# Optimization experiments

Hardware: AMD Instinct MI355X
Metric: run time of the kernel (lower is better)

The kernel has to match this reference:

```python
import jax, jax.numpy as jnp
import numpy as np

N, F = 4096, 256  # nodes, in_features == hidden_features == out_features; num_heads = 1
LN_EPS = 1e-5
L1_EPS = 1e-12


def setup_inputs() -> dict:
    key = jax.random.key(0)
    k0, k1, k2, k3, k4 = jax.random.split(key, 5)
    h = jax.random.normal(k0, (N, F), jnp.float32)
    x = jax.random.normal(k1, (N, F), jnp.float32)
    s = 1.0 / np.sqrt(F)
    s_v = 1.0 / np.sqrt(F + 3)
    # torch Linear weight layout: [out_features, in_features]
    w_k = jax.random.uniform(k2, (F, F), jnp.float32, -s, s)
    w_q = jax.random.uniform(k3, (F, F), jnp.float32, -s, s)
    w_v = jax.random.uniform(k4, (F, F + 3), jnp.float32, -s_v, s_v)
    # mixing init: ones * semantic_weight(-1.0), row 0 zeroed
    mixing = jnp.full((2, 2), -1.0, jnp.float32).at[0].set(0.0)
    ln_gamma = jnp.ones((F,), jnp.float32)
    ln_beta = jnp.zeros((F,), jnp.float32)
    return {"h": h, "x": x, "w_k": w_k, "w_q": w_q, "w_v": w_v,
            "mixing": mixing, "ln_gamma": ln_gamma, "ln_beta": ln_beta}


def reference(h, x, w_k, w_q, w_v, mixing, ln_gamma, ln_beta):
    h0, x0 = h, x
    # LayerNorm (biased variance, eps=1e-5)
    mu = h.mean(-1, keepdims=True)
    var = ((h - mu) ** 2).mean(-1, keepdims=True)
    hn = (h - mu) * jax.lax.rsqrt(var + LN_EPS) * ln_gamma + ln_beta
    # F.normalize(x, p=1): divide by max(L1 norm, eps)
    xn = x / jnp.maximum(jnp.abs(x).sum(-1, keepdims=True), L1_EPS)
    # projections (single head: [N, F])
    k = hn @ w_k.T
    q = hn @ w_q.T
    # feature-attention: softmax over last dim of k q^T / sqrt(F)
    a_h = jax.nn.softmax((k @ q.T) * (F ** -0.5), axis=-1)          # [N, N]
    # x-affinity
    a_x = xn @ xn.T                                                  # [N, N]
    # stats of a_x rows: diag, sum, std (unbiased, ddof=1)
    i = jnp.stack([jnp.diagonal(a_x), a_x.sum(-1), a_x.std(-1, ddof=1)], axis=-1)  # [N, 3]
    # learned 2x2 mixing, softmax over dim 0 (columns)
    m = jax.nn.softmax(mixing, axis=0)
    a_x2 = a_x * m[0, 0] + a_h * m[1, 0]
    a_h2 = a_x * m[0, 1] + a_h * m[1, 1]
    # torch a_h.transpose(-1, 0) swaps the row axis with the head axis,
    # transposing the NxN matrix (head dim = 1): h <- a_h2^T @ hn
    h_agg = a_h2.T @ hn                                              # [N, F]
    x_out = a_x2 @ xn                                                # [N, F]
    h_out = jax.nn.elu(jnp.concatenate([h_agg, i], axis=-1) @ w_v.T)
    return (h_out + h0, x_out + x0)
```

## Files before the change

### kernel.cpp

```cpp
#include <hip/hip_runtime.h>
#include <cstdint>
#include <cstddef>

#define NB 4096
#define FD 256

typedef __attribute__((ext_vector_type(4))) float f32x4;
typedef __attribute__((ext_vector_type(8))) short bf16x8;

__device__ __forceinline__ ushort f2bf(float f) {
  union { float f; uint32_t u; } v; v.f = f;
  uint32_t r = v.u + 0x7fffu + ((v.u >> 16) & 1u);
  return (ushort)(r >> 16);
}
__device__ __forceinline__ float bf2f(ushort b) {
  union { uint32_t u; float f; } v; v.u = ((uint32_t)b) << 16;
  return v.f;
}

__device__ __forceinline__ void gld16(const void* g, void* l) {
  __builtin_amdgcn_global_load_lds(
      (const __attribute__((address_space(1))) char*)g,
      (__attribute__((address_space(3))) char*)l, 16, 0, 0);
}

__device__ __forceinline__ float wave_reduce_sum(float v) {
#pragma unroll
  for (int off = 32; off >= 1; off >>= 1) v += __shfl_xor(v, off);
  return v;
}
__device__ __forceinline__ float wave_reduce_max(float v) {
#pragma unroll
  for (int off = 32; off >= 1; off >>= 1) v = fmaxf(v, __shfl_xor(v, off));
  return v;
}

__global__ __launch_bounds__(256) void rownorm_wcast_kernel(
    const float* __restrict__ h, const float* __restrict__ x,
    const float* __restrict__ gamma, const float* __restrict__ beta,
    ushort* __restrict__ hnb, ushort* __restrict__ xnb, float* __restrict__ diag,
    const float* __restrict__ w_k, const float* __restrict__ w_q,
    const float* __restrict__ w_v,
    ushort* __restrict__ wkqb, ushort* __restrict__ wvAb,
    float* __restrict__ wvbT3) {
  __shared__ float rA[4], rB[4], rC[4], rD[4];
  if (blockIdx.x >= NB) {
    const int r = blockIdx.x - NB, t = threadIdx.x;
    wkqb[r * 256 + t] = f2bf(w_k[r * 256 + t]);
    wkqb[(256 + r) * 256 + t] = f2bf(w_q[r * 256 + t]);
    wvAb[r * 256 + t] = f2bf(w_v[(size_t)r * 259 + t]);
    if (t < 3) wvbT3[t * 256 + r] = w_v[(size_t)r * 259 + 256 + t];
    return;
  }
  const int r = blockIdx.x, t = threadIdx.x, wid = t >> 6, lane = t & 63;
  const size_t base = (size_t)r * FD + t;
  const float hv = h[base], xv = x[base];
  float s1 = wave_reduce_sum(hv);
  float s2 = wave_reduce_sum(hv * hv);
  float a1 = wave_reduce_sum(fabsf(xv));
  float q1 = wave_reduce_sum(xv * xv);
  if (lane == 0) { rA[wid] = s1; rB[wid] = s2; rC[wid] = a1; rD[wid] = q1; }
  __syncthreads();
  const float S1 = rA[0] + rA[1] + rA[2] + rA[3];
  const float S2 = rB[0] + rB[1] + rB[2] + rB[3];
  const float L1 = rC[0] + rC[1] + rC[2] + rC[3];
  const float Q1 = rD[0] + rD[1] + rD[2] + rD[3];
  const float mu = S1 * (1.0f / FD);
  const float var = S2 * (1.0f / FD) - mu * mu;
  const float rstd = rsqrtf(var + 1e-5f);
  const float d = fmaxf(L1, 1e-12f), dinv = 1.0f / d;
  hnb[base] = f2bf((hv - mu) * rstd * gamma[t] + beta[t]);
  xnb[base] = f2bf(xv * dinv);
  if (t == 0) diag[r] = Q1 * dinv * dinv;
}

__global__ __launch_bounds__(256) void transpose2_kernel(
    const ushort* __restrict__ inA, ushort* __restrict__ outA,
    const ushort* __restrict__ inB, ushort* __restrict__ outB, int R, int C) {
  __shared__ ushort tile[64][65];
  const ushort* in = blockIdx.z ? inB : inA;
  ushort* out = blockIdx.z ? outB : outA;
  const int bc = blockIdx.x * 64, br = blockIdx.y * 64;
  const int t = threadIdx.x;
#pragma unroll
  for (int i = 0; i < 16; ++i) {
    const int idx = t + 256 * i;
    const int rr = idx >> 6, cc = idx & 63;
    tile[rr][cc] = in[(size_t)(br + rr) * C + bc + cc];
  }
  __syncthreads();
#pragma unroll
  for (int i = 0; i < 16; ++i) {
    const int idx = t + 256 * i;
    const int rr = idx >> 6, cc = idx & 63;
    out[(size_t)(bc + rr) * R + br + cc] = tile[cc][rr];
  }
}

__global__ __launch_bounds__(256) void transpose4_kernel(
    const ushort* __restrict__ in, ushort* __restrict__ out, int R, int C) {
  __shared__ ushort tile[64][66];
  const int bc = blockIdx.x * 64, br = blockIdx.y * 64;
  const int t = threadIdx.x;
  const int c4 = (t & 15) * 4;
  const int r0 = t >> 4;
#pragma unroll
  for (int i = 0; i < 4; ++i) {
    const int rr = r0 + 16 * i;
    *(ushort4*)&tile[rr][c4] =
        *(const ushort4*)(in + (size_t)(br + rr) * C + bc + c4);
  }
  __syncthreads();
#pragma unroll
  for (int i = 0; i < 4; ++i) {
    const int ro = r0 + 16 * i;
    ushort4 o;
    o.x = tile[c4 + 0][ro];
    o.y = tile[c4 + 1][ro];
    o.z = tile[c4 + 2][ro];
    o.w = tile[c4 + 3][ro];
    *(ushort4*)(out + (size_t)(bc + ro) * R + br + c4) = o;
  }
}

__global__ __launch_bounds__(256) void colsum_kernel(
    const ushort* __restrict__ xnT, float* __restrict__ s) {
  __shared__ float red[4];
  const int f = blockIdx.x, t = threadIdx.x, wid = t >> 6, lane = t & 63;
  float a = 0.f;
#pragma unroll
  for (int i = 0; i < 16; ++i) a += bf2f(xnT[(size_t)f * NB + t + 256 * i]);
  a = wave_reduce_sum(a);
  if (lane == 0) red[wid] = a;
  __syncthreads();
  if (t == 0) s[f] = red[0] + red[1] + red[2] + red[3];
}

__global__ __launch_bounds__(256) void reduce16g_kernel(
    const float* __restrict__ in, ushort* __restrict__ t23B,
    ushort* __restrict__ M2T) {
  const int idx = blockIdx.x * 256 + threadIdx.x;
  const int i = idx >> 9, j = idx & 511;
  float a = 0.f;
#pragma unroll
  for (int z = 0; z < 16; ++z) a += in[(size_t)z * (256 * 512) + idx];
  if (j < 256) t23B[i * 256 + j] = f2bf(a);
  else M2T[i * 256 + (j - 256)] = f2bf(a);
}

__global__ __launch_bounds__(256) void softmax_kernel(
    const ushort* __restrict__ S, ushort* __restrict__ P) {
  __shared__ float red[4];
  const int r = blockIdx.x, t = threadIdx.x, wid = t >> 6, lane = t & 63;
  const uint4* Sr = (const uint4*)(S + (size_t)r * NB);
  float v[16];
  float lmax = -1e30f;
#pragma unroll
  for (int i = 0; i < 2; ++i) {
    const uint4 c = Sr[t + 256 * i];
    const uint32_t w4[4] = {c.x, c.y, c.z, c.w};
#pragma unroll
    for (int j = 0; j < 4; ++j) {
      v[i * 8 + j * 2]     = bf2f((ushort)(w4[j] & 0xffffu));
      v[i * 8 + j * 2 + 1] = bf2f((ushort)(w4[j] >> 16));
    }
  }
#pragma unroll
  for (int u = 0; u < 16; ++u) lmax = fmaxf(lmax, v[u]);
  lmax = wave_reduce_max(lmax);
  if (lane == 0) red[wid] = lmax;
  __syncthreads();
  const float gmax = fmaxf(fmaxf(red[0], red[1]), fmaxf(red[2], red[3]));
  __syncthreads();
  float lsum = 0.f;
#pragma unroll
  for (int u = 0; u < 16; ++u) { v[u] = __expf(v[u] - gmax); lsum += v[u]; }
  lsum = wave_reduce_sum(lsum);
  if (lane == 0) red[wid] = lsum;
  __syncthreads();
  const float pinv = 1.f / (red[0] + red[1] + red[2] + red[3]);
  uint4* Pr = (uint4*)(P + (size_t)r * NB);
#pragma unroll
  for (int i = 0; i < 2; ++i) {
    uint4 o;
    o.x = (uint32_t)f2bf(v[i*8+0] * pinv) | ((uint32_t)f2bf(v[i*8+1] * pinv) << 16);
    o.y = (uint32_t)f2bf(v[i*8+2] * pinv) | ((uint32_t)f2bf(v[i*8+3] * pinv) << 16);
    o.z = (uint32_t)f2bf(v[i*8+4] * pinv) | ((uint32_t)f2bf(v[i*8+5] * pinv) << 16);
    o.w = (uint32_t)f2bf(v[i*8+6] * pinv) | ((uint32_t)f2bf(v[i*8+7] * pinv) << 16);
    Pr[t + 256 * i] = o;
  }
}

__global__ __launch_bounds__(256) void megacombine_kernel(
    const ushort* __restrict__ px, const ushort* __restrict__ ph,
    const float* __restrict__ t23, const ushort* __restrict__ xnb,
    const float* __restrict__ sv, const float* __restrict__ diag,
    const float* __restrict__ x, const float* __restrict__ h,
    const float* __restrict__ wvbT3, const float* __restrict__ mix,
    float* __restrict__ out_x, float* __restrict__ out_h) {
  __shared__ float rA[4], rB[4];
  const size_t NF = (size_t)NB * FD;
  const int i = blockIdx.x, f = threadIdx.x, wid = f >> 6, lane = f & 63;
  const float e0x = __expf(mix[0]), e1x = __expf(mix[2]);
  const float mAx = e0x / (e0x + e1x), mBx = e1x / (e0x + e1x);
  const float e0h = __expf(mix[1]), e1h = __expf(mix[3]);
  const float mAh = e0h / (e0h + e1h), mBh = e1h / (e0h + e1h);

  const size_t rowoff = (size_t)i * FD + f;
  float ax = 0.f, ah = 0.f;
#pragma unroll
  for (int z = 0; z < 4; ++z) {
    ax += bf2f(px[(size_t)z * NF + rowoff]);
    ah += bf2f(ph[(size_t)z * NF + rowoff]);
  }
  const float t2v = t23[(size_t)i * 512 + f];
  const float t3v = t23[(size_t)i * 512 + 256 + f];
  const float xv = bf2f(xnb[rowoff]);

  float rs = wave_reduce_sum(xv * sv[f]);
  float rq = wave_reduce_sum(xv * t2v);
  if (lane == 0) { rA[wid] = rs; rB[wid] = rq; }
  __syncthreads();
  rs = rA[0] + rA[1] + rA[2] + rA[3];
  rq = rB[0] + rB[1] + rB[2] + rB[3];
  const float mean = rs * (1.0f / NB);
  const float var = (rq - (float)NB * mean * mean) * (1.0f / (NB - 1));
  const float sd = sqrtf(fmaxf(var, 0.f));
  const float dg = diag[i];
  const float statsterm = dg * wvbT3[f] + rs * wvbT3[256 + f] + sd * wvbT3[512 + f];

  out_x[rowoff] = mBx * ax + mAx * t2v + x[rowoff];
  const float pre = mBh * ah + mAh * t3v + statsterm;
  out_h[rowoff] = ((pre > 0.f) ? pre : expm1f(pre)) + h[rowoff];
}

struct GDesc {
  const ushort* A; const ushort* B; void* C;
  int lda, ldb, ldc, K, gx, gy, epi;
  float alpha; long pstride; int nb;
};

__global__ __launch_bounds__(256) void gemm_batch3(
    GDesc d0, GDesc d1, GDesc d2, int ntot) {
  int flat = blockIdx.x;
  flat = (flat & 7) * (ntot >> 3) + (flat >> 3);
  GDesc d; int l;
  if (flat < d0.nb) { d = d0; l = flat; }
  else if (flat < d0.nb + d1.nb) { d = d1; l = flat - d0.nb; }
  else { d = d2; l = flat - d0.nb - d1.nb; }
  const int bx = l % d.gx;
  const int rest = l / d.gx;
  const int by = rest % d.gy, bz = rest / d.gy;

  __shared__ __align__(16) ushort At[2][64][32];
  __shared__ __align__(16) ushort Bt[2][64][32];
  const int tid = threadIdx.x;
  const int wave = tid >> 6, lane = tid & 63;
  const int wr = wave >> 1, wc = wave & 1;
  const int bi = by * 64, bj = bx * 64;
  const int fr = lane & 15, fq = lane >> 4;
  const int sub = lane >> 2, q = lane & 3;

  f32x4 acc[2][2];
#pragma unroll
  for (int m = 0; m < 2; ++m)
#pragma unroll
    for (int n = 0; n < 2; ++n) acc[m][n] = (f32x4){0.f, 0.f, 0.f, 0.f};

  const int kbase = bz * d.K;
  const int kend = kbase + d.K;

  auto stage = [&](int bufi, int k0) {
    {
      const int row = wave * 16 + sub;
      const int qs = q ^ (row & 3);
      gld16(d.A + (size_t)(bi + row) * d.lda + k0 + qs * 8, &At[bufi][wave * 16][0]);
    }
    {
      const int row = wave * 16 + sub;
      const int qs = q ^ (row & 3);
      gld16(d.B + (size_t)(bj + row) * d.ldb + k0 + qs * 8, &Bt[bufi][wave * 16][0]);
    }
  };

  stage(0, kbase);
  __syncthreads();

  int cur = 0;
  for (int k0 = kbase; k0 < kend; k0 += 32) {
    if (k0 + 32 < kend) stage(cur ^ 1, k0 + 32);
    bf16x8 a[2], b[2];
#pragma unroll
    for (int m = 0; m < 2; ++m) {
      const int row = wr * 32 + m * 16 + fr;
      a[m] = *(const bf16x8*)((const char*)&At[cur][row][0] + ((fq ^ (row & 3)) * 16));
    }
#pragma unroll
    for (int n = 0; n < 2; ++n) {
      const int row = wc * 32 + n * 16 + fr;
      b[n] = *(const bf16x8*)((const char*)&Bt[cur][row][0] + ((fq ^ (row & 3)) * 16));
    }
#pragma unroll
    for (int m = 0; m < 2; ++m)
#pragma unroll
      for (int n = 0; n < 2; ++n)
        acc[m][n] = __builtin_amdgcn_mfma_f32_16x16x32_bf16(a[m], b[n], acc[m][n], 0, 0, 0);
    __syncthreads();
    cur ^= 1;
  }

#pragma unroll
  for (int m = 0; m < 2; ++m)
#pragma unroll
    for (int n = 0; n < 2; ++n)
#pragma unroll
      for (int r = 0; r < 4; ++r) {
        const int row = bi + wr * 32 + m * 16 + fq * 4 + r;
        const int col = bj + wc * 32 + n * 16 + fr;
        const size_t ci = (size_t)row * d.ldc + col;
        const float v = acc[m][n][r];
        if (d.epi == 1) ((ushort*)d.C)[ci] = f2bf(v * d.alpha);
        else ((float*)d.C)[(size_t)bz * d.pstride + ci] = v;
      }
}

#define GEMM128_BODY(APTR, BPTR, LDA, LDB, KBASE, KEND)                        \
  f32x4 acc[4][4];                                                             \
  _Pragma("unroll") for (int m = 0; m < 4; ++m)                                \
      _Pragma("unroll") for (int n = 0; n < 4; ++n)                            \
          acc[m][n] = (f32x4){0.f, 0.f, 0.f, 0.f};                             \
  auto stage = [&](int bufi, int k0) {                                         \
    for (int c = wave; c < 16; c += 4) {                                       \
      const int row = c * 8 + sub8;                                            \
      const int qs = q8 ^ (row & 7);                                           \
      gld16(APTR + (size_t)(bi + row) * LDA + k0 + qs * 8, &At[bufi][c * 8][0]); \
    }                                                                          \
    for (int c = wave; c < 16; c += 4) {                                       \
      const int row = c * 8 + sub8;                                            \
      const int qs = q8 ^ (row & 7);                                           \
      gld16(BPTR + (size_t)(bj + row) * LDB + k0 + qs * 8, &Bt[bufi][c * 8][0]); \
    }                                                                          \
  };                                                                           \
  stage(0, KBASE);                                                             \
  __syncthreads();                                                             \
  int cur = 0;                                                                 \
  for (int k0 = KBASE; k0 < KEND; k0 += 64) {                                  \
    if (k0 + 64 < KEND) stage(cur ^ 1, k0 + 64);                               \
    _Pragma("unroll") for (int ks = 0; ks < 2; ++ks) {                         \
      bf16x8 a[4], b[4];                                                       \
      _Pragma("unroll") for (int m = 0; m < 4; ++m) {                          \
        const int row = wr * 64 + m * 16 + fr;                                 \
        const int ch = (ks * 4 + fq) ^ (row & 7);                              \
        a[m] = *(const bf16x8*)((const char*)&At[cur][row][0] + ch * 16);      \
      }                                                                        \
      _Pragma("unroll") for (int n = 0; n < 4; ++n) {                          \
        const int row = wc * 64 + n * 16 + fr;                                 \
        const int ch = (ks * 4 + fq) ^ (row & 7);                              \
        b[n] = *(const bf16x8*)((const char*)&Bt[cur][row][0] + ch * 16);      \
      }                                                                        \
      _Pragma("unroll") for (int m = 0; m < 4; ++m)                            \
          _Pragma("unroll") for (int n = 0; n < 4; ++n)                        \
              acc[m][n] = __builtin_amdgcn_mfma_f32_16x16x32_bf16(             \
                  a[m], b[n], acc[m][n], 0, 0, 0);                             \
    }                                                                          \
    __syncthreads();                                                           \
    cur ^= 1;                                                                  \
  }

__global__ __launch_bounds__(256) void gemm_agg(
    const ushort* __restrict__ P, const ushort* __restrict__ PT,
    const ushort* __restrict__ xnT, const ushort* __restrict__ hvT,
    ushort* __restrict__ px, ushort* __restrict__ ph) {
  __shared__ __align__(16) ushort At[2][128][64];
  __shared__ __align__(16) ushort Bt[2][128][64];
  const int tid = threadIdx.x;
  const int wave = tid >> 6, lane = tid & 63;
  const int wr = wave >> 1, wc = wave & 1;

  const int nwg = 512;
  int flat = blockIdx.x + 2 * (blockIdx.y + 32 * blockIdx.z);
  flat = (flat & 7) * (nwg >> 3) + (flat >> 3);
  const int bx = flat % 2, by = (flat / 2) % 32, bz = flat / 64;
  const int sel = bz >> 2, kz = bz & 3;

  const ushort* A = sel ? PT : P;
  const ushort* B = sel ? hvT : xnT;
  ushort* C = sel ? ph : px;

  const int bi = by * 128, bj = bx * 128;
  const int fr = lane & 15, fq = lane >> 4;
  const int sub8 = lane >> 3, q8 = lane & 7;

  const int kbase = kz * 1024;
  const int kend = kbase + 1024;

  GEMM128_BODY(A, B, NB, NB, kbase, kend)

#pragma unroll
  for (int m = 0; m < 4; ++m)
#pragma unroll
    for (int n = 0; n < 4; ++n)
#pragma unroll
      for (int r = 0; r < 4; ++r) {
        const int row = bi + wr * 64 + m * 16 + fq * 4 + r;
        const int col = bj + wc * 64 + n * 16 + fr;
        C[(size_t)kz * ((size_t)NB * FD) + (size_t)row * FD + col] = f2bf(acc[m][n][r]);
      }
}

struct GD2 {
  const ushort* A; const ushort* B; void* C;
  int lda, ldb, ldc, K, gx, epi;
  float alpha; int nb;
};

__global__ __launch_bounds__(256) void gemm_batch2big(GD2 d0, GD2 d1, int ntot) {
  __shared__ __align__(16) ushort At[2][128][64];
  __shared__ __align__(16) ushort Bt[2][128][64];
  const int tid = threadIdx.x;
  const int wave = tid >> 6, lane = tid & 63;
  const int wr = wave >> 1, wc = wave & 1;

  int flat = blockIdx.x;
  flat = (flat & 7) * (ntot >> 3) + (flat >> 3);
  GD2 d; int l;
  if (flat < d0.nb) { d = d0; l = flat; }
  else { d = d1; l = flat - d0.nb; }
  const int bx = l % d.gx, by = l / d.gx;

  const int bi = by * 128, bj = bx * 128;
  const int fr = lane & 15, fq = lane >> 4;
  const int sub8 = lane >> 3, q8 = lane & 7;

  GEMM128_BODY(d.A, d.B, d.lda, d.ldb, 0, d.K)

#pragma unroll
  for (int m = 0; m < 4; ++m)
#pragma unroll
    for (int n = 0; n < 4; ++n)
#pragma unroll
      for (int r = 0; r < 4; ++r) {
        const int row = bi + wr * 64 + m * 16 + fq * 4 + r;
        const int col = bj + wc * 64 + n * 16 + fr;
        const size_t ci = (size_t)row * d.ldc + col;
        const float v = acc[m][n][r];
        if (d.epi == 1) ((ushort*)d.C)[ci] = f2bf(v * d.alpha);
        else ((float*)d.C)[ci] = v;
      }
}

template <int BM, int BN, int EPI>
__global__ __launch_bounds__(256) void gemm_nt(
    const ushort* __restrict__ A, int lda,
    const ushort* __restrict__ B, int ldb,
    void* __restrict__ Cp, int ldc, int K, float alpha,
    size_t pstride) {
  constexpr int WAVES_N = 2, WAVES_M = 2;
  constexpr int WM = BM / WAVES_M, WN = BN / WAVES_N;
  constexpr int MR = WM / 16, NR = WN / 16;
  __shared__ __align__(16) ushort At[2][BM][32];
  __shared__ __align__(16) ushort Bt[2][BN][32];
  const int tid = threadIdx.x;
  const int wave = tid >> 6, lane = tid & 63;
  const int wr = wave / WAVES_N, wc = wave % WAVES_N;

  const int bx = blockIdx.x, by = blockIdx.y;
  const int bi = by * BM, bj = bx * BN;
  const int fr = lane & 15, fq = lane >> 4;
  const int sub = lane >> 2, q = lane & 3;

  f32x4 acc[MR][NR];
#pragma unroll
  for (int m = 0; m < MR; ++m)
#pragma unroll
    for (int n = 0; n < NR; ++n) acc[m][n] = (f32x4){0.f, 0.f, 0.f, 0.f};

  auto stage = [&](int bufi, int k0) {
    for (int c = wave; c < BM / 16; c += 4) {
      const int row = c * 16 + sub;
      const int qs = q ^ (row & 3);
      gld16(A + (size_t)(bi + row) * lda + k0 + qs * 8, &At[bufi][c * 16][0]);
    }
    for (int c = wave; c < BN / 16; c += 4) {
      const int row = c * 16 + sub;
      const int qs = q ^ (row & 3);
      gld16(B + (size_t)(bj + row) * ldb + k0 + qs * 8, &Bt[bufi][c * 16][0]);
    }
  };

  stage(0, 0);
  __syncthreads();

  int cur = 0;
  for (int k0 = 0; k0 < K; k0 += 32) {
    if (k0 + 32 < K) stage(cur ^ 1, k0 + 32);
    bf16x8 a[MR], b[NR];
#pragma unroll
    for (int m = 0; m < MR; ++m) {
      const int row = wr * WM + m * 16 + fr;
      a[m] = *(const bf16x8*)((const char*)&At[cur][row][0] + ((fq ^ (row & 3)) * 16));
    }
#pragma unroll
    for (int n = 0; n < NR; ++n) {
      const int row = wc * WN + n * 16 + fr;
      b[n] = *(const bf16x8*)((const char*)&Bt[cur][row][0] + ((fq ^ (row & 3)) * 16));
    }
#pragma unroll
    for (int m = 0; m < MR; ++m)
#pragma unroll
      for (int n = 0; n < NR; ++n)
        acc[m][n] = __builtin_amdgcn_mfma_f32_16x16x32_bf16(a[m], b[n], acc[m][n], 0, 0, 0);
    __syncthreads();
    cur ^= 1;
  }

#pragma unroll
  for (int m = 0; m < MR; ++m)
#pragma unroll
    for (int n = 0; n < NR; ++n)
#pragma unroll
      for (int r = 0; r < 4; ++r) {
        const int row = bi + wr * WM + m * 16 + fq * 4 + r;
        const int col = bj + wc * WN + n * 16 + fr;
        const size_t ci = (size_t)row * ldc + col;
        const float v = acc[m][n][r];
        if (EPI == 0) ((float*)Cp)[ci] = v * alpha;
        else ((ushort*)Cp)[ci] = f2bf(v * alpha);
      }
}

extern "C" void kernel_launch(void* const* d_in, const int* in_sizes, int n_in,
                              void* d_out, int out_size, void* d_ws, size_t ws_size,
                              hipStream_t stream) {
  const float* h      = (const float*)d_in[0];
  const float* x      = (const float*)d_in[1];
  const float* w_k    = (const float*)d_in[2];
  const float* w_q    = (const float*)d_in[3];
  const float* w_v    = (const float*)d_in[4];
  const float* mixing = (const float*)d_in[5];
  const float* gamma  = (const float*)d_in[6];
  const float* beta   = (const float*)d_in[7];

  float* out_h = (float*)d_out;
  float* out_x = out_h + (size_t)NB * FD;

  char* w = (char*)d_ws;
  ushort* S     = (ushort*)(w + 0);
  ushort* P     = (ushort*)(w + 33554432);
  ushort* PT    = (ushort*)(w + 67108864);
  ushort* hnb   = (ushort*)(w + 100663296);
  ushort* xnb   = (ushort*)(w + 102760448);
  ushort* xnbT  = (ushort*)(w + 104857600);
  ushort* hnbT  = (ushort*)(w + 106954752);
  ushort* kq    = (ushort*)(w + 109051904);
  ushort* hvT   = (ushort*)(w + 113246208);
  float*  t23   = (float*)(w + 115343360);
  ushort* t23B  = (ushort*)(w + 123731968);
  ushort* M2T   = (ushort*)(w + 123994112);
  ushort* wkqb  = (ushort*)(w + 124125184);
  ushort* wvAb  = (ushort*)(w + 124387328);
  float*  wvbT3 = (float*)(w + 124518400);
  float*  diag  = (float*)(w + 124521472);
  float*  sv    = (float*)(w + 124537856);
  float*  Gramp = (float*)(w + 67108864);
  ushort* px    = (ushort*)(w + 0);
  ushort* ph    = (ushort*)(w + 16777216);

  rownorm_wcast_kernel<<<NB + FD, 256, 0, stream>>>(
      h, x, gamma, beta, hnb, xnb, diag, w_k, w_q, w_v, wkqb, wvAb, wvbT3);
  transpose2_kernel<<<dim3(FD / 64, NB / 64, 2), 256, 0, stream>>>(
      xnb, xnbT, hnb, hnbT, NB, FD);
  colsum_kernel<<<FD, 256, 0, stream>>>(xnbT, sv);

  {
    GDesc dkq = {hnb, wkqb, kq, FD, FD, 512, FD, 8, 64, 1, 1.f, 0, 512};
    GDesc dgr = {xnbT, xnbT, Gramp, NB, NB, 512, NB / 16, 8, 4, 5, 1.f,
                 (long)(256 * 512), 512};
    GDesc dhv = {wvAb, hnb, hvT, FD, FD, NB, FD, 64, 4, 1, 1.f, 0, 256};
    gemm_batch3<<<1280, 256, 0, stream>>>(dkq, dgr, dhv, 1280);
  }
  reduce16g_kernel<<<256 * 512 / 256, 256, 0, stream>>>(Gramp, t23B, M2T);

  gemm_nt<64, 64, 1><<<dim3(4, 4), 256, 0, stream>>>(
      wvAb, FD, M2T, FD, t23B + 256 * 256, FD, FD, 1.f, 0);

  {
    GD2 dS  = {kq, kq + 256, S, 512, 512, NB, FD, 32, 1, 0.0625f, 1024};
    GD2 dT  = {xnb, t23B, t23, FD, FD, 512, FD, 4, 0, 1.f, 128};
    gemm_batch2big<<<1152, 256, 0, stream>>>(dS, dT, 1152);
  }

  softmax_kernel<<<NB, 256, 0, stream>>>(S, P);
  transpose4_kernel<<<dim3(NB / 64, NB / 64), 256, 0, stream>>>(P, PT, NB, NB);

  gemm_agg<<<dim3(2, 32, 8), 256, 0, stream>>>(P, PT, xnbT, hvT, px, ph);

  megacombine_kernel<<<NB, 256, 0, stream>>>(
      px, ph, t23, xnb, sv, diag, x, h, wvbT3, mixing, out_x, out_h);
}
```

Before: 117.7 us.

## Fold column-sum into batched GEMM launch and double K-step per stage

```diff
diff --git a/kernel.cpp b/kernel.cpp
--- a/kernel.cpp
+++ b/kernel.cpp
@@ -123,19 +123,6 @@
   }
 }
 
-__global__ __launch_bounds__(256) void colsum_kernel(
-    const ushort* __restrict__ xnT, float* __restrict__ s) {
-  __shared__ float red[4];
-  const int f = blockIdx.x, t = threadIdx.x, wid = t >> 6, lane = t & 63;
-  float a = 0.f;
-#pragma unroll
-  for (int i = 0; i < 16; ++i) a += bf2f(xnT[(size_t)f * NB + t + 256 * i]);
-  a = wave_reduce_sum(a);
-  if (lane == 0) red[wid] = a;
-  __syncthreads();
-  if (t == 0) s[f] = red[0] + red[1] + red[2] + red[3];
-}
-
 __global__ __launch_bounds__(256) void reduce16g_kernel(
     const float* __restrict__ in, ushort* __restrict__ t23B,
     ushort* __restrict__ M2T) {
@@ -240,10 +227,26 @@
   float alpha; long pstride; int nb;
 };
 
-__global__ __launch_bounds__(256) void gemm_batch3(
-    GDesc d0, GDesc d1, GDesc d2, int ntot) {
+__global__ __launch_bounds__(256) void gemm_batch4(
+    GDesc d0, GDesc d1, GDesc d2,
+    const ushort* __restrict__ xnT, float* __restrict__ sv, int ntot) {
   int flat = blockIdx.x;
   flat = (flat & 7) * (ntot >> 3) + (flat >> 3);
+  const int ngemm = d0.nb + d1.nb + d2.nb;
+
+  if (flat >= ngemm) {
+    __shared__ float red[4];
+    const int f = flat - ngemm, t = threadIdx.x, wid = t >> 6, lane = t & 63;
+    float a = 0.f;
+#pragma unroll
+    for (int i = 0; i < 16; ++i) a += bf2f(xnT[(size_t)f * NB + t + 256 * i]);
+    a = wave_reduce_sum(a);
+    if (lane == 0) red[wid] = a;
+    __syncthreads();
+    if (t == 0) sv[f] = red[0] + red[1] + red[2] + red[3];
+    return;
+  }
+
   GDesc d; int l;
   if (flat < d0.nb) { d = d0; l = flat; }
   else if (flat < d0.nb + d1.nb) { d = d1; l = flat - d0.nb; }
@@ -252,14 +255,14 @@
   const int rest = l / d.gx;
   const int by = rest % d.gy, bz = rest / d.gy;
 
-  __shared__ __align__(16) ushort At[2][64][32];
-  __shared__ __align__(16) ushort Bt[2][64][32];
+  __shared__ __align__(16) ushort At[2][64][64];
+  __shared__ __align__(16) ushort Bt[2][64][64];
   const int tid = threadIdx.x;
   const int wave = tid >> 6, lane = tid & 63;
   const int wr = wave >> 1, wc = wave & 1;
   const int bi = by * 64, bj = bx * 64;
   const int fr = lane & 15, fq = lane >> 4;
-  const int sub = lane >> 2, q = lane & 3;
+  const int sub8 = lane >> 3, q8 = lane & 7;
 
   f32x4 acc[2][2];
 #pragma unroll
@@ -271,15 +274,15 @@
   const int kend = kbase + d.K;
 
   auto stage = [&](int bufi, int k0) {
-    {
-      const int row = wave * 16 + sub;
-      const int qs = q ^ (row & 3);
-      gld16(d.A + (size_t)(bi + row) * d.lda + k0 + qs * 8, &At[bufi][wave * 16][0]);
-    }
-    {
-      const int row = wave * 16 + sub;
-      const int qs = q ^ (row & 3);
-      gld16(d.B + (size_t)(bj + row) * d.ldb + k0 + qs * 8, &Bt[bufi][wave * 16][0]);
+    for (int c = wave; c < 8; c += 4) {
+      const int row = c * 8 + sub8;
+      const int qs = q8 ^ (row & 7);
+      gld16(d.A + (size_t)(bi + row) * d.lda + k0 + qs * 8, &At[bufi][c * 8][0]);
+    }
+    for (int c = wave; c < 8; c += 4) {
+      const int row = c * 8 + sub8;
+      const int qs = q8 ^ (row & 7);
+      gld16(d.B + (size_t)(bj + row) * d.ldb + k0 + qs * 8, &Bt[bufi][c * 8][0]);
     }
   };
 
@@ -287,24 +290,29 @@
   __syncthreads();
 
   int cur = 0;
-  for (int k0 = kbase; k0 < kend; k0 += 32) {
-    if (k0 + 32 < kend) stage(cur ^ 1, k0 + 32);
-    bf16x8 a[2], b[2];
-#pragma unroll
-    for (int m = 0; m < 2; ++m) {
-      const int row = wr * 32 + m * 16 + fr;
-      a[m] = *(const bf16x8*)((const char*)&At[cur][row][0] + ((fq ^ (row & 3)) * 16));
-    }
-#pragma unroll
-    for (int n = 0; n < 2; ++n) {
-      const int row = wc * 32 + n * 16 + fr;
-      b[n] = *(const bf16x8*)((const char*)&Bt[cur][row][0] + ((fq ^ (row & 3)) * 16));
-    }
-#pragma unroll
-    for (int m = 0; m < 2; ++m)
-#pragma unroll
-      for (int n = 0; n < 2; ++n)
-        acc[m][n] = __builtin_amdgcn_mfma_f32_16x16x32_bf16(a[m], b[n], acc[m][n], 0, 0, 0);
+  for (int k0 = kbase; k0 < kend; k0 += 64) {
+    if (k0 + 64 < kend) stage(cur ^ 1, k0 + 64);
+#pragma unroll
+    for (int ks = 0; ks < 2; ++ks) {
+      bf16x8 a[2], b[2];
+#pragma unroll
+      for (int m = 0; m < 2; ++m) {
+        const int row = wr * 32 + m * 16 + fr;
+        const int ch = (ks * 4 + fq) ^ (row & 7);
+        a[m] = *(const bf16x8*)((const char*)&At[cur][row][0] + ch * 16);
+      }
+#pragma unroll
+      for (int n = 0; n < 2; ++n) {
+        const int row = wc * 32 + n * 16 + fr;
+        const int ch = (ks * 4 + fq) ^ (row & 7);
+        b[n] = *(const bf16x8*)((const char*)&Bt[cur][row][0] + ch * 16);
+      }
+#pragma unroll
+      for (int m = 0; m < 2; ++m)
+#pragma unroll
+        for (int n = 0; n < 2; ++n)
+          acc[m][n] = __builtin_amdgcn_mfma_f32_16x16x32_bf16(a[m], b[n], acc[m][n], 0, 0, 0);
+    }
     __syncthreads();
     cur ^= 1;
   }
@@ -570,14 +578,13 @@
       h, x, gamma, beta, hnb, xnb, diag, w_k, w_q, w_v, wkqb, wvAb, wvbT3);
   transpose2_kernel<<<dim3(FD / 64, NB / 64, 2), 256, 0, stream>>>(
       xnb, xnbT, hnb, hnbT, NB, FD);
-  colsum_kernel<<<FD, 256, 0, stream>>>(xnbT, sv);
 
   {
     GDesc dkq = {hnb, wkqb, kq, FD, FD, 512, FD, 8, 64, 1, 1.f, 0, 512};
     GDesc dgr = {xnbT, xnbT, Gramp, NB, NB, 512, NB / 16, 8, 4, 5, 1.f,
                  (long)(256 * 512), 512};
     GDesc dhv = {wvAb, hnb, hvT, FD, FD, NB, FD, 64, 4, 1, 1.f, 0, 256};
-    gemm_batch3<<<1280, 256, 0, stream>>>(dkq, dgr, dhv, 1280);
+    gemm_batch4<<<1536, 256, 0, stream>>>(dkq, dgr, dhv, xnbT, sv, 1536);
   }
   reduce16g_kernel<<<256 * 512 / 256, 256, 0, stream>>>(Gramp, t23B, M2T);
 
```

Result: no change. 116.8 us (-0.7%).
